# Kernel tuning notes

Measured on AMD Instinct MI355X. Metric: run time of the kernel, lower is better.

Reference implementation:

```python
import jax, jax.numpy as jnp
import numpy as np

BETA = 6.0
LOG_2PI = float(np.log(2.0 * np.pi))


def setup_inputs() -> dict:
    key = jax.random.key(0)
    k1, k2, k3, k4 = jax.random.split(key, 4)
    B, L = 2048, 64
    kl = jax.random.uniform(k1, (B, L), dtype=jnp.float32)
    z_mean = jax.random.normal(k2, (B, L), dtype=jnp.float32)
    z_logvar = jax.random.normal(k3, (B, L), dtype=jnp.float32)
    z_sampled = jax.random.normal(k4, (B, L), dtype=jnp.float32)
    return {"kl": kl, "z_mean": z_mean, "z_logvar": z_logvar, "z_sampled": z_sampled}


def gaussian_log_density(samples, mean, log_var):
    # samples: [B,1,L], mean/log_var: [1,B,L] -> [B,B,L]
    tmp = samples - mean
    return -0.5 * (tmp * tmp * jnp.exp(-log_var) + log_var + LOG_2PI)


def total_correlation(z, z_mean, z_logvar):
    # [B, B, L]: log q(z_i_l | x_j)
    log_qz_prob = gaussian_log_density(z[:, None, :], z_mean[None, :, :], z_logvar[None, :, :])
    # sum_l logsumexp_j -> [B]
    log_qz_product = jnp.sum(jax.scipy.special.logsumexp(log_qz_prob, axis=1), axis=1)
    # logsumexp_j sum_l -> [B]
    log_qz = jax.scipy.special.logsumexp(jnp.sum(log_qz_prob, axis=2), axis=1)
    return jnp.mean(log_qz - log_qz_product)


def reference(kl, z_mean, z_logvar, z_sampled):
    kl_loss = jnp.sum(kl)
    tc = (BETA - 1.0) * total_correlation(z_sampled, z_mean, z_logvar)
    return tc + kl_loss
```

## Files before the change

kernel.cpp:

```cpp
#include <hip/hip_runtime.h>
#include <math.h>


#define NB 2048
#define NL 64
#define NE (NB * NL)
#define BVAL 12.0f

__device__ __forceinline__ float wredsum(float v) {
#pragma unroll
  for (int o = 32; o; o >>= 1) v += __shfl_xor(v, o, 64);
  return v;
}
__device__ __forceinline__ float wredmax(float v) {
#pragma unroll
  for (int o = 32; o; o >>= 1) v = fmaxf(v, __shfl_xor(v, o, 64));
  return v;
}

__global__ __launch_bounds__(256) void k1_pre(const float* __restrict__ kl,
                                              const float* __restrict__ zm,
                                              const float* __restrict__ zlv,
                                              float4* __restrict__ PK2,
                                              float* __restrict__ A2T,
                                              float* __restrict__ MA2T,
                                              float* __restrict__ QC2,
                                              float* __restrict__ KLP) {
  const float INVLN2 = 1.4426950408889634f;
  const float LOG2PI = 1.8378770664093453f;
  int tid = threadIdx.x;
  int e = blockIdx.x * 256 + tid;
  int j = e >> 6, l = e & 63;
  float lv = zlv[e], m = zm[e];
  float a2 = -0.5f * INVLN2 * __expf(-lv);
  float b2 = -0.5f * INVLN2 * (lv + LOG2PI);
  float c1 = -2.0f * a2 * m;
  float c0 = fmaf(a2 * m, m, b2);
  PK2[e] = make_float4(a2, c1, c0 - BVAL, 0.0f);
  A2T[l * NB + j] = a2;
  MA2T[l * NB + j] = c1;
  float q = wredsum(c0);
  if (l == 0) QC2[j] = q;
  float ks = wredsum(kl[e]);
  __shared__ float sk[4];
  if (l == 0) sk[tid >> 6] = ks;
  __syncthreads();
  if (tid == 0) KLP[blockIdx.x] = sk[0] + sk[1] + sk[2] + sk[3];
}

__global__ __launch_bounds__(256) void k2_t(const float* __restrict__ zs,
                                            const float* __restrict__ A2T,
                                            const float* __restrict__ MA2T,
                                            const float* __restrict__ QC2,
                                            float* __restrict__ TPM,
                                            float* __restrict__ TPS) {
  int jc = blockIdx.x;
  int i0 = blockIdx.y * 8;
  int tid = threadIdx.x;
  int w = tid >> 6;
  int j = jc * 256 + tid;
  __shared__ float zsh[64][8];
  if (tid < 128) {
    int k = tid >> 1, r0 = (tid & 1) * 4;
#pragma unroll
    for (int r = 0; r < 4; ++r) zsh[k][r0 + r] = zs[(i0 + r0 + r) * NL + k];
  }
  __syncthreads();
  float accv[8];
  float q = QC2[j];
#pragma unroll
  for (int r = 0; r < 8; ++r) accv[r] = q;
  for (int k = 0; k < 64; ++k) {
    float av = A2T[k * NB + j];
    float mv = MA2T[k * NB + j];
    const float4* z4 = (const float4*)&zsh[k][0];
    float4 za = z4[0], zb = z4[1];
    float zk[8] = {za.x, za.y, za.z, za.w, zb.x, zb.y, zb.z, zb.w};
#pragma unroll
    for (int r = 0; r < 8; ++r) {
      accv[r] = fmaf(zk[r] * zk[r], av, accv[r]);
      accv[r] = fmaf(zk[r], mv, accv[r]);
    }
  }
  __shared__ float lm[4][8], ls[4][8];
#pragma unroll
  for (int r = 0; r < 8; ++r) {
    float mx = wredmax(accv[r]);
    if ((tid & 63) == 0) lm[w][r] = mx;
  }
  __syncthreads();
  float Mt[8];
#pragma unroll
  for (int r = 0; r < 8; ++r)
    Mt[r] = fmaxf(fmaxf(lm[0][r], lm[1][r]), fmaxf(lm[2][r], lm[3][r]));
#pragma unroll
  for (int r = 0; r < 8; ++r) {
    float ss = wredsum(__builtin_amdgcn_exp2f(accv[r] - Mt[r]));
    if ((tid & 63) == 0) ls[w][r] = ss;
  }
  __syncthreads();
  if (tid == 0) {
#pragma unroll
    for (int r = 0; r < 8; ++r) {
      TPM[(i0 + r) * 8 + jc] = Mt[r];
      TPS[(i0 + r) * 8 + jc] = ls[0][r] + ls[1][r] + ls[2][r] + ls[3][r];
    }
  }
}

__global__ __launch_bounds__(256) void k3_lse(const float* __restrict__ zs,
                                              const float4* __restrict__ PK2,
                                              float* __restrict__ SP) {
  int jc = blockIdx.x;
  int i0 = blockIdx.y * 8;
  int tid = threadIdx.x;
  int w = tid >> 6, l = tid & 63;
  const float4* p = PK2 + (size_t)(jc * 256 + w * 64) * NL + l;
  float zr[8];
#pragma unroll
  for (int r = 0; r < 8; ++r) zr[r] = zs[(i0 + r) * NL + l];
  float S[8];
#pragma unroll
  for (int r = 0; r < 8; ++r) S[r] = 0.0f;
#pragma unroll 4
  for (int jj = 0; jj < 64; ++jj) {
    float4 c = p[(size_t)jj * NL];
#pragma unroll
    for (int r = 0; r < 8; ++r) {
      float lp2 = fmaf(fmaf(zr[r], c.x, c.y), zr[r], c.z);
      S[r] += __builtin_amdgcn_exp2f(lp2);
    }
  }
  __shared__ float lss[4][8][64];
#pragma unroll
  for (int r = 0; r < 8; ++r) lss[w][r][l] = S[r];
  __syncthreads();
  for (int pp = tid; pp < 512; pp += 256) {
    int r = pp >> 6, ll = pp & 63;
    float Sc = lss[0][r][ll] + lss[1][r][ll] + lss[2][r][ll] + lss[3][r][ll];
    SP[((size_t)jc * NB + (i0 + r)) * NL + ll] = Sc;
  }
}

__global__ __launch_bounds__(256) void k4_fin(const float* __restrict__ SP,
                                              const float* __restrict__ TPM,
                                              const float* __restrict__ TPS,
                                              float* __restrict__ PERI) {
  int tid = threadIdx.x;
  int w = tid >> 6, l = tid & 63;
  int i = blockIdx.x * 4 + w;
  float S = 0.0f;
#pragma unroll
  for (int s = 0; s < 8; ++s) S += SP[((size_t)s * NB + i) * NL + l];
  float val = __builtin_amdgcn_logf(S);
  float lqp2 = wredsum(val) + 64.0f * BVAL;
  float tm = (l < 8) ? TPM[i * 8 + l] : -1e30f;
  float ts = (l < 8) ? TPS[i * 8 + l] : 0.0f;
  float Mt = wredmax(tm);
  float St = wredsum(ts * __builtin_amdgcn_exp2f(tm - Mt));
  float lqz2 = Mt + __builtin_amdgcn_logf(St);
  if (l == 0) PERI[i] = lqz2 - lqp2;
}

__global__ __launch_bounds__(256) void k5_out(const float* __restrict__ KLP,
                                              const float* __restrict__ PERI,
                                              float* __restrict__ out) {
  int tid = threadIdx.x;
  float a = 0.0f, b = 0.0f;
  for (int x = tid; x < 512; x += 256) a += KLP[x];
  for (int x = tid; x < 2048; x += 256) b += PERI[x];
  float ra = wredsum(a), rb = wredsum(b);
  __shared__ float sa[4], sb[4];
  if ((tid & 63) == 0) {
    sa[tid >> 6] = ra;
    sb[tid >> 6] = rb;
  }
  __syncthreads();
  if (tid == 0) {
    const float LN2 = 0.6931471805599453f;
    float ka = sa[0] + sa[1] + sa[2] + sa[3];
    float kb = sb[0] + sb[1] + sb[2] + sb[3];
    out[0] = ka + 5.0f * LN2 * kb * (1.0f / (float)NB);
  }
}

extern "C" void kernel_launch(void* const* d_in, const int* in_sizes, int n_in,
                              void* d_out, int out_size, void* d_ws, size_t ws_size,
                              hipStream_t stream) {
  const float* kl = (const float*)d_in[0];
  const float* zm = (const float*)d_in[1];
  const float* zlv = (const float*)d_in[2];
  const float* zs = (const float*)d_in[3];
  float* ws = (float*)d_ws;

  float* PK2 = ws;
  float* A2T = PK2 + 4 * NE;
  float* MA2T = A2T + NE;
  float* QC2 = MA2T + NE;
  float* SP = QC2 + NB;
  float* TPM = SP + 8 * NE;
  float* TPS = TPM + NB * 8;
  float* KLP = TPS + NB * 8;
  float* PERI = KLP + 512;

  k1_pre<<<NE / 256, 256, 0, stream>>>(kl, zm, zlv, (float4*)PK2, A2T, MA2T, QC2, KLP);
  k2_t<<<dim3(8, NB / 8), 256, 0, stream>>>(zs, A2T, MA2T, QC2, TPM, TPS);
  k3_lse<<<dim3(8, NB / 8), 256, 0, stream>>>(zs, (const float4*)PK2, SP);
  k4_fin<<<NB / 4, 256, 0, stream>>>(SP, TPM, TPS, PERI);
  k5_out<<<1, 256, 0, stream>>>(KLP, PERI, (float*)d_out);
}
```

Measured before the change: 132.7 us.

## Fuse five kernels into three with atomic accumulation and last-block reduction

Merges the TC logsumexp kernel and the per-dimension sum-of-exp kernel into one kernel that shares the block index and staged z data. The per-chunk partial buffer is replaced with a zeroed accumulator updated by float atomicAdd. The final output reduction is folded into the finish kernel with a last-block counter pattern. This removes two launches and a large partial-sum write/read, at the cost of atomic contention, nondeterministic summation order, and larger per-block register and shared-memory use in the fused kernel.

```diff
diff --git a/kernel.cpp b/kernel.cpp
--- a/kernel.cpp
+++ b/kernel.cpp
@@ -18,14 +18,16 @@
   return v;
 }
 
-__global__ __launch_bounds__(256) void k1_pre(const float* __restrict__ kl,
+__global__ __launch_bounds__(256) void ka_pre(const float* __restrict__ kl,
                                               const float* __restrict__ zm,
                                               const float* __restrict__ zlv,
                                               float4* __restrict__ PK2,
                                               float* __restrict__ A2T,
                                               float* __restrict__ MA2T,
                                               float* __restrict__ QC2,
-                                              float* __restrict__ KLP) {
+                                              float* __restrict__ KLP,
+                                              float* __restrict__ Sacc,
+                                              int* __restrict__ CNT) {
   const float INVLN2 = 1.4426950408889634f;
   const float LOG2PI = 1.8378770664093453f;
   int tid = threadIdx.x;
@@ -39,6 +41,7 @@
   PK2[e] = make_float4(a2, c1, c0 - BVAL, 0.0f);
   A2T[l * NB + j] = a2;
   MA2T[l * NB + j] = c1;
+  Sacc[e] = 0.0f;
   float q = wredsum(c0);
   if (l == 0) QC2[j] = q;
   float ks = wredsum(kl[e]);
@@ -46,19 +49,23 @@
   if (l == 0) sk[tid >> 6] = ks;
   __syncthreads();
   if (tid == 0) KLP[blockIdx.x] = sk[0] + sk[1] + sk[2] + sk[3];
-}
-
-__global__ __launch_bounds__(256) void k2_t(const float* __restrict__ zs,
-                                            const float* __restrict__ A2T,
-                                            const float* __restrict__ MA2T,
-                                            const float* __restrict__ QC2,
-                                            float* __restrict__ TPM,
-                                            float* __restrict__ TPS) {
-  int jc = blockIdx.x;
-  int i0 = blockIdx.y * 8;
+  if (blockIdx.x == 0 && tid == 0) *CNT = 0;
+}
+
+__global__ __launch_bounds__(256, 8) void kb_main(const float* __restrict__ zs,
+                                                  const float* __restrict__ A2T,
+                                                  const float* __restrict__ MA2T,
+                                                  const float* __restrict__ QC2,
+                                                  const float4* __restrict__ PK2,
+                                                  float* __restrict__ TPM,
+                                                  float* __restrict__ TPS,
+                                                  float* __restrict__ Sacc) {
+  int bid = blockIdx.x;
+  int jc = bid & 7;
+  int i0 = (bid >> 3) * 8;
   int tid = threadIdx.x;
-  int w = tid >> 6;
-  int j = jc * 256 + tid;
+  int w = tid >> 6, l = tid & 63;
+
   __shared__ float zsh[64][8];
   if (tid < 128) {
     int k = tid >> 1, r0 = (tid & 1) * 4;
@@ -66,6 +73,7 @@
     for (int r = 0; r < 4; ++r) zsh[k][r0 + r] = zs[(i0 + r0 + r) * NL + k];
   }
   __syncthreads();
+  int j = jc * 256 + tid;
   float accv[8];
   float q = QC2[j];
 #pragma unroll
@@ -86,7 +94,7 @@
 #pragma unroll
   for (int r = 0; r < 8; ++r) {
     float mx = wredmax(accv[r]);
-    if ((tid & 63) == 0) lm[w][r] = mx;
+    if (l == 0) lm[w][r] = mx;
   }
   __syncthreads();
   float Mt[8];
@@ -96,7 +104,7 @@
 #pragma unroll
   for (int r = 0; r < 8; ++r) {
     float ss = wredsum(__builtin_amdgcn_exp2f(accv[r] - Mt[r]));
-    if ((tid & 63) == 0) ls[w][r] = ss;
+    if (l == 0) ls[w][r] = ss;
   }
   __syncthreads();
   if (tid == 0) {
@@ -106,15 +114,7 @@
       TPS[(i0 + r) * 8 + jc] = ls[0][r] + ls[1][r] + ls[2][r] + ls[3][r];
     }
   }
-}
-
-__global__ __launch_bounds__(256) void k3_lse(const float* __restrict__ zs,
-                                              const float4* __restrict__ PK2,
-                                              float* __restrict__ SP) {
-  int jc = blockIdx.x;
-  int i0 = blockIdx.y * 8;
-  int tid = threadIdx.x;
-  int w = tid >> 6, l = tid & 63;
+
   const float4* p = PK2 + (size_t)(jc * 256 + w * 64) * NL + l;
   float zr[8];
 #pragma unroll
@@ -138,20 +138,21 @@
   for (int pp = tid; pp < 512; pp += 256) {
     int r = pp >> 6, ll = pp & 63;
     float Sc = lss[0][r][ll] + lss[1][r][ll] + lss[2][r][ll] + lss[3][r][ll];
-    SP[((size_t)jc * NB + (i0 + r)) * NL + ll] = Sc;
-  }
-}
-
-__global__ __launch_bounds__(256) void k4_fin(const float* __restrict__ SP,
+    atomicAdd(&Sacc[(size_t)(i0 + r) * NL + ll], Sc);
+  }
+}
+
+__global__ __launch_bounds__(256) void kc_fin(const float* __restrict__ Sacc,
                                               const float* __restrict__ TPM,
                                               const float* __restrict__ TPS,
-                                              float* __restrict__ PERI) {
+                                              const float* __restrict__ KLP,
+                                              float* __restrict__ PERB,
+                                              int* __restrict__ CNT,
+                                              float* __restrict__ out) {
   int tid = threadIdx.x;
   int w = tid >> 6, l = tid & 63;
   int i = blockIdx.x * 4 + w;
-  float S = 0.0f;
-#pragma unroll
-  for (int s = 0; s < 8; ++s) S += SP[((size_t)s * NB + i) * NL + l];
+  float S = Sacc[(size_t)i * NL + l];
   float val = __builtin_amdgcn_logf(S);
   float lqp2 = wredsum(val) + 64.0f * BVAL;
   float tm = (l < 8) ? TPM[i * 8 + l] : -1e30f;
@@ -159,21 +160,28 @@
   float Mt = wredmax(tm);
   float St = wredsum(ts * __builtin_amdgcn_exp2f(tm - Mt));
   float lqz2 = Mt + __builtin_amdgcn_logf(St);
-  if (l == 0) PERI[i] = lqz2 - lqp2;
-}
-
-__global__ __launch_bounds__(256) void k5_out(const float* __restrict__ KLP,
-                                              const float* __restrict__ PERI,
-                                              float* __restrict__ out) {
-  int tid = threadIdx.x;
+  __shared__ float sblk[4];
+  if (l == 0) sblk[w] = lqz2 - lqp2;
+  __syncthreads();
+  __shared__ int slast;
+  if (tid == 0) {
+    float v = sblk[0] + sblk[1] + sblk[2] + sblk[3];
+    __hip_atomic_store(&PERB[blockIdx.x], v, __ATOMIC_RELEASE, __HIP_MEMORY_SCOPE_AGENT);
+    int old = __hip_atomic_fetch_add(CNT, 1, __ATOMIC_ACQ_REL, __HIP_MEMORY_SCOPE_AGENT);
+    slast = (old == 511) ? 1 : 0;
+  }
+  __syncthreads();
+  if (!slast) return;
   float a = 0.0f, b = 0.0f;
-  for (int x = tid; x < 512; x += 256) a += KLP[x];
-  for (int x = tid; x < 2048; x += 256) b += PERI[x];
+  for (int x = tid; x < 512; x += 256) {
+    a += KLP[x];
+    b += __hip_atomic_load(&PERB[x], __ATOMIC_ACQUIRE, __HIP_MEMORY_SCOPE_AGENT);
+  }
   float ra = wredsum(a), rb = wredsum(b);
   __shared__ float sa[4], sb[4];
-  if ((tid & 63) == 0) {
-    sa[tid >> 6] = ra;
-    sb[tid >> 6] = rb;
+  if (l == 0) {
+    sa[w] = ra;
+    sb[w] = rb;
   }
   __syncthreads();
   if (tid == 0) {
@@ -197,15 +205,16 @@
   float* A2T = PK2 + 4 * NE;
   float* MA2T = A2T + NE;
   float* QC2 = MA2T + NE;
-  float* SP = QC2 + NB;
-  float* TPM = SP + 8 * NE;
+  float* Sacc = QC2 + NB;
+  float* TPM = Sacc + NE;
   float* TPS = TPM + NB * 8;
   float* KLP = TPS + NB * 8;
-  float* PERI = KLP + 512;
-
-  k1_pre<<<NE / 256, 256, 0, stream>>>(kl, zm, zlv, (float4*)PK2, A2T, MA2T, QC2, KLP);
-  k2_t<<<dim3(8, NB / 8), 256, 0, stream>>>(zs, A2T, MA2T, QC2, TPM, TPS);
-  k3_lse<<<dim3(8, NB / 8), 256, 0, stream>>>(zs, (const float4*)PK2, SP);
-  k4_fin<<<NB / 4, 256, 0, stream>>>(SP, TPM, TPS, PERI);
-  k5_out<<<1, 256, 0, stream>>>(KLP, PERI, (float*)d_out);
-}
+  float* PERB = KLP + 512;
+  int* CNT = (int*)(PERB + 512);
+
+  ka_pre<<<NE / 256, 256, 0, stream>>>(kl, zm, zlv, (float4*)PK2, A2T, MA2T, QC2,
+                                       KLP, Sacc, CNT);
+  kb_main<<<2048, 256, 0, stream>>>(zs, A2T, MA2T, QC2, (const float4*)PK2, TPM,
+                                    TPS, Sacc);
+  kc_fin<<<512, 256, 0, stream>>>(Sacc, TPM, TPS, KLP, PERB, CNT, (float*)d_out);
+}
```

After: 139.2 us. +4.9%, slower.
